# Kernel tuning notes

Measured on AMD Instinct MI355X. Metric: run time of the kernel, lower is better.

The kernel has to match this reference:

```python
import jax, jax.numpy as jnp
import numpy as np

N_HEAD = 16
D_HEAD = 64  # d_model=1024 // n_head=16


def setup_inputs() -> dict:
    key = jax.random.key(0)
    ks = jax.random.split(key, 8)
    B, S, D = 2, 2048, 1024
    scale = 1.0 / np.sqrt(D)
    return {
        "q": jax.random.normal(ks[0], (B, S, D), jnp.float32),
        "k": jax.random.normal(ks[1], (B, S, D), jnp.float32),
        "v": jax.random.normal(ks[2], (B, S, D), jnp.float32),
        "w_q": jax.random.normal(ks[3], (D, D), jnp.float32) * scale,
        "w_k": jax.random.normal(ks[4], (D, D), jnp.float32) * scale,
        "w_v": jax.random.normal(ks[5], (D, D), jnp.float32) * scale,
        "w_fc": jax.random.normal(ks[6], (D, D), jnp.float32) * scale,
        "b_fc": jnp.zeros((D,), jnp.float32),
    }


def reference(q, k, v, w_q, w_k, w_v, w_fc, b_fc):
    B, Sq, D = q.shape
    # projections (torch Linear: x @ W.T), split into heads -> [B, H, S, Dh]
    def proj(x, w):
        return (x @ w.T).reshape(B, x.shape[1], N_HEAD, D_HEAD).transpose(0, 2, 1, 3)
    qh, kh, vh = proj(q, w_q), proj(k, w_k), proj(v, w_v)
    # scaled dot-product attention with explicit weights (dropout = identity, eval mode)
    scores = jnp.einsum("bhqd,bhkd->bhqk", qh, kh) / jnp.sqrt(jnp.float32(D_HEAD))
    attn = jax.nn.softmax(scores, axis=-1)  # [B, H, Sq, Sk]
    ctx = jnp.einsum("bhqk,bhkd->bhqd", attn, vh)
    ctx = ctx.transpose(0, 2, 1, 3).reshape(B, Sq, D)
    out = ctx @ w_fc.T + b_fc
    return out, attn
```

## Files before the change

kernel.cpp:

```cpp
#include <hip/hip_runtime.h>


using f16   = _Float16;
using f16x4 = __attribute__((ext_vector_type(4))) f16;
using f16x8 = __attribute__((ext_vector_type(8))) f16;
using f32x4 = __attribute__((ext_vector_type(4))) float;

#define MFMA16(a, b, c) __builtin_amdgcn_mfma_f32_16x16x32_f16((a), (b), (c), 0, 0, 0)

__device__ static inline float fexp2(float x) {
#if __has_builtin(__builtin_amdgcn_exp2f)
  return __builtin_amdgcn_exp2f(x);
#else
  return exp2f(x);
#endif
}

#define C1 0.18033688011112042f

#define WAIT_BARRIER(IMM)                                              \
  do {                                                                 \
    asm volatile("s_waitcnt vmcnt(" #IMM ") lgkmcnt(0)" ::: "memory"); \
    __builtin_amdgcn_s_barrier();                                      \
  } while (0)

__device__ static inline void gld16(const void* gptr, void* lptr) {
  __builtin_amdgcn_global_load_lds(
      (const __attribute__((address_space(1))) void*)gptr,
      (__attribute__((address_space(3))) void*)lptr, 16, 0, 0);
}

__device__ static inline unsigned int pack2(float a, float b) {
  union { f16 h[2]; unsigned int u; } x;
  x.h[0] = (f16)a; x.h[1] = (f16)b;
  return x.u;
}

__global__ __launch_bounds__(256) void cast_all(
    const float* __restrict__ q, const float* __restrict__ k,
    const float* __restrict__ v, const float* __restrict__ wq,
    const float* __restrict__ wk, const float* __restrict__ wv,
    const float* __restrict__ wfc, f16* __restrict__ ws) {
  int i = blockIdx.x * 256 + threadIdx.x;
  const float* src;
  f16* dst;
  int li;
  if (i < 3145728) {
    if (i < 1048576)      { src = q; dst = ws;            li = i; }
    else if (i < 2097152) { src = k; dst = ws + 4194304;  li = i - 1048576; }
    else                  { src = v; dst = ws + 8388608;  li = i - 2097152; }
  } else {
    int j = i - 3145728;
    int wsel = j >> 18;
    src = (wsel == 0) ? wq : (wsel == 1) ? wk : (wsel == 2) ? wv : wfc;
    dst = ws + 12582912 + wsel * 1048576;
    li = j & 262143;
  }
  float4 x = ((const float4*)src)[li];
  f16x4 y;
  y[0] = (f16)x.x; y[1] = (f16)x.y; y[2] = (f16)x.z; y[3] = (f16)x.w;
  ((f16x4*)dst)[li] = y;
}

template <int MODE, int BN>
__global__ __launch_bounds__(256) void gemm_bt(
    const f16* __restrict__ A0, const f16* __restrict__ W0,
    const float* __restrict__ bias, void* __restrict__ Cout) {
  constexpr int FJ = BN / 32;
  __shared__ unsigned short XA[8192];
  __shared__ unsigned short WB2[BN * 64];
  int tid = threadIdx.x;
  int w = tid >> 6, l = tid & 63, lq = l & 15, g = l >> 4;
  int nb3 = blockIdx.x * BN, mb = blockIdx.y * 128;
  int wsel = (MODE == 4) ? (nb3 >> 10) : 0;
  int nb = (MODE == 4) ? (nb3 & 1023) : nb3;
  const f16* A = (MODE == 4) ? A0 + (size_t)wsel * 4194304 : A0;
  const f16* W = (MODE == 4) ? W0 + (size_t)wsel * 1048576 : W0;
  bool swapR = (MODE == 4) && (wsel == 2);
  int wi = w >> 1, wj = w & 1;

  f32x4 acc[4][FJ];
#pragma unroll
  for (int i = 0; i < 4; i++)
#pragma unroll
    for (int j = 0; j < FJ; j++) acc[i][j] = (f32x4){0.f, 0.f, 0.f, 0.f};

  char* Xb = (char*)XA;
  char* Wb = (char*)WB2;
  int row = tid >> 3;
  int c = (tid & 7) ^ (row & 7);
  const f16* Asrc = A + (size_t)(mb + row) * 1024 + c * 8;
  const f16* Wsrc = W + (size_t)(nb + row) * 1024 + c * 8;

  for (int k0 = 0; k0 < 1024; k0 += 64) {
#pragma unroll
    for (int i2 = 0; i2 < 4; i2++)
      gld16(Asrc + k0 + i2 * 32 * 1024, Xb + i2 * 4096 + w * 1024);
#pragma unroll
    for (int i2 = 0; i2 < BN / 32; i2++)
      gld16(Wsrc + k0 + i2 * 32 * 1024, Wb + i2 * 4096 + w * 1024);
    __syncthreads();

    const char* at = swapR ? Wb : Xb;
    const char* bt = swapR ? Xb : Wb;

    f16x8 bfr[FJ][2];
#pragma unroll
    for (int f = 0; f < FJ; f++) {
      int r = wj * (BN / 2) + f * 16 + lq;
      int sw = (r & 7) << 4;
      bfr[f][0] = *(const f16x8*)(bt + r * 128 + ((g * 16) ^ sw));
      bfr[f][1] = *(const f16x8*)(bt + r * 128 + ((64 + g * 16) ^ sw));
    }
#pragma unroll
    for (int fi = 0; fi < 4; fi++) {
      int r = wi * 64 + fi * 16 + lq;
      int sw = (r & 7) << 4;
      f16x8 a0 = *(const f16x8*)(at + r * 128 + ((g * 16) ^ sw));
      f16x8 a1 = *(const f16x8*)(at + r * 128 + ((64 + g * 16) ^ sw));
#pragma unroll
      for (int fj = 0; fj < FJ; fj++) {
        acc[fi][fj] = MFMA16(a0, bfr[fj][0], acc[fi][fj]);
        acc[fi][fj] = MFMA16(a1, bfr[fj][1], acc[fi][fj]);
      }
    }
    __syncthreads();
  }

#pragma unroll
  for (int fi = 0; fi < 4; fi++) {
#pragma unroll
    for (int fj = 0; fj < FJ; fj++) {
#pragma unroll
      for (int jj = 0; jj < 4; jj++) {
        float v = acc[fi][fj][jj];
        int iG = (swapR ? nb : mb) + wi * 64 + fi * 16 + g * 4 + jj;
        int jG = (swapR ? mb : nb) + wj * (BN / 2) + fj * 16 + lq;
        if constexpr (MODE == 3) {
          int m2 = iG, n2 = jG;
          ((float*)Cout)[(size_t)m2 * 1024 + n2] = v + bias[n2];
        } else {
          f16* dstb = (f16*)Cout + (size_t)wsel * 4194304;
          if (!swapR) {
            int m2 = iG, n2 = jG;
            size_t dst = (size_t)((m2 >> 11) * 16 + (n2 >> 6)) * 131072 +
                         (size_t)(m2 & 2047) * 64 + (n2 & 63);
            dstb[dst] = (f16)v;
          } else {
            int n2 = iG, m2 = jG;
            size_t dst = (size_t)((m2 >> 11) * 1024 + n2) * 2048 + (m2 & 2047);
            dstb[dst] = (f16)v;
          }
        }
      }
    }
  }
}

__global__ __launch_bounds__(256, 2) void attn_fused(
    const f16* __restrict__ qh, const f16* __restrict__ kh,
    const f16* __restrict__ vt, float* __restrict__ attn,
    f16* __restrict__ ctx) {
  __shared__ unsigned short Kl[3][4096];
  __shared__ unsigned short Vl[3][4096];
  __shared__ unsigned short Pl[16384];
  int tid = threadIdx.x;
  int w = tid >> 6, l = tid & 63, lq = l & 15, g = l >> 4;

  int bid = blockIdx.x;
  int xcd = bid & 7, j = bid >> 3;
  int bh = xcd * 4 + (j >> 4);
  int qt = j & 15;

  const f16* qbase = qh + (size_t)(bh * 2048 + qt * 128 + w * 32 + lq) * 64;
  f16x8 qf[2][2];
#pragma unroll
  for (int f = 0; f < 2; f++) {
    qf[f][0] = *(const f16x8*)(qbase + f * 16 * 64 + g * 8);
    qf[f][1] = *(const f16x8*)(qbase + f * 16 * 64 + 32 + g * 8);
  }
  asm volatile("s_waitcnt vmcnt(0)" ::: "memory");

  char* Kb = (char*)Kl;
  char* Vb = (char*)Vl;
  char* Pw = (char*)Pl + w * 8192;

  int row = tid >> 3;
  int c = (tid & 7) ^ (row & 7);
  const f16* ksrc = kh + (size_t)bh * 131072 + (size_t)row * 64 + c * 8;
  const f16* vsrc = vt + (size_t)bh * 131072 + (size_t)row * 2048 + c * 8;

  int swq = (lq & 7) << 4;

#define KISSUE(i, b_)                                               \
  do {                                                              \
    const f16* kp_ = ksrc + (size_t)(i) * 4096;                     \
    char* kb_ = Kb + (b_) * 8192;                                   \
    gld16(kp_, kb_ + w * 1024);                                     \
    gld16(kp_ + 2048, kb_ + 4096 + w * 1024);                       \
  } while (0)
#define VISSUE(i, b_)                                               \
  do {                                                              \
    const f16* vp_ = vsrc + (size_t)(i) * 64;                       \
    char* vb_ = Vb + (b_) * 8192;                                   \
    gld16(vp_, vb_ + w * 1024);                                     \
    gld16(vp_ + 32 * 2048, vb_ + 4096 + w * 1024);                  \
  } while (0)

  float ls[2] = {0.f, 0.f};
  KISSUE(0, 0);
  WAIT_BARRIER(0);
  for (int t = 0; t < 32; t++) {
    if (t < 31) KISSUE(t + 1, (t + 1) & 1);
    const char* KbC = Kb + (t & 1) * 8192;
#pragma unroll
    for (int cf = 0; cf < 4; cf++) {
      int kr = cf * 16 + lq;
      int sw = (kr & 7) << 4;
      f16x8 ka  = *(const f16x8*)(KbC + kr * 128 + ((g * 16) ^ sw));
      f16x8 kb2 = *(const f16x8*)(KbC + kr * 128 + ((64 + g * 16) ^ sw));
#pragma unroll
      for (int f = 0; f < 2; f++) {
        f32x4 s = (f32x4){0.f, 0.f, 0.f, 0.f};
        s = MFMA16(ka, qf[f][0], s);
        s = MFMA16(kb2, qf[f][1], s);
        ls[f] += fexp2(s[0] * C1) + fexp2(s[1] * C1) +
                 fexp2(s[2] * C1) + fexp2(s[3] * C1);
      }
    }
    WAIT_BARRIER(0);
  }
  float linv[2];
#pragma unroll
  for (int f = 0; f < 2; f++) {
    float t2 = ls[f];
    t2 += __shfl_xor(t2, 16);
    t2 += __shfl_xor(t2, 32);
    linv[f] = 1.0f / t2;
  }

  f32x4 acc[2][4];
#pragma unroll
  for (int f = 0; f < 2; f++)
#pragma unroll
    for (int i = 0; i < 4; i++) acc[f][i] = (f32x4){0.f, 0.f, 0.f, 0.f};

  float* attnw =
      attn + ((size_t)bh * 2048 + qt * 128 + w * 32) * 2048;

  int rsub = l >> 5;
  int c4 = (l & 31) * 4;
  int sb = c4 * 2;
  int shalf = sb & 128;
  int slocal = sb & 127;

  KISSUE(0, 0); VISSUE(0, 0);
  KISSUE(1, 1); VISSUE(1, 1);
  WAIT_BARRIER(4);
  int bc = 0;
  for (int t = 0; t < 32; t++) {
    int bn = bc + 2; if (bn >= 3) bn -= 3;
    if (t + 2 < 32) { KISSUE(t + 2, bn); VISSUE(t + 2, bn); }
    const char* KbC = Kb + bc * 8192;
    const char* VbC = Vb + bc * 8192;
    int hb = (t & 1) * 128;

#pragma unroll
    for (int cf = 0; cf < 4; cf++) {
      int kr = cf * 16 + lq;
      int sw = (kr & 7) << 4;
      f16x8 ka  = *(const f16x8*)(KbC + kr * 128 + ((g * 16) ^ sw));
      f16x8 kb2 = *(const f16x8*)(KbC + kr * 128 + ((64 + g * 16) ^ sw));
      int k0 = cf * 16 + g * 4;
#pragma unroll
      for (int f = 0; f < 2; f++) {
        f32x4 s = (f32x4){0.f, 0.f, 0.f, 0.f};
        s = MFMA16(ka, qf[f][0], s);
        s = MFMA16(kb2, qf[f][1], s);
        float e0 = fexp2(s[0] * C1) * linv[f];
        float e1 = fexp2(s[1] * C1) * linv[f];
        float e2 = fexp2(s[2] * C1) * linv[f];
        float e3 = fexp2(s[3] * C1) * linv[f];
        char* Pr = Pw + (f * 16 + lq) * 256 + hb;
        *(unsigned int*)(Pr + ((k0 * 2) ^ swq))       = pack2(e0, e1);
        *(unsigned int*)(Pr + (((k0 + 2) * 2) ^ swq)) = pack2(e2, e3);
      }
    }

    {
      f16x8 pb[2][2];
#pragma unroll
      for (int f = 0; f < 2; f++) {
        char* Pr = Pw + (f * 16 + lq) * 256 + hb;
        pb[f][0] = *(const f16x8*)(Pr + ((g * 16) ^ swq));
        pb[f][1] = *(const f16x8*)(Pr + ((64 + g * 16) ^ swq));
      }
#pragma unroll
      for (int af = 0; af < 4; af++) {
        int vr = af * 16 + lq;
        int sv = (vr & 7) << 4;
        f16x8 va0 = *(const f16x8*)(VbC + vr * 128 + ((g * 16) ^ sv));
        f16x8 va1 = *(const f16x8*)(VbC + vr * 128 + ((64 + g * 16) ^ sv));
#pragma unroll
        for (int f = 0; f < 2; f++) {
          acc[f][af] = MFMA16(va0, pb[f][0], acc[f][af]);
          acc[f][af] = MFMA16(va1, pb[f][1], acc[f][af]);
        }
      }
    }

    if (t & 1) {
      float* abase = attnw + (t - 1) * 64 + c4;
#pragma unroll
      for (int i = 0; i < 16; i++) {
        int r = i * 2 + rsub;
        f16x4 pv = *(const f16x4*)(Pw + r * 256 + shalf +
                                   (slocal ^ ((r & 7) << 4)));
        float4 o = {(float)pv[0], (float)pv[1], (float)pv[2], (float)pv[3]};
        *(float4*)(abase + (size_t)r * 2048) = o;
      }
    }

    if (t == 0)      { WAIT_BARRIER(4);  }
    else if (t >= 30){ WAIT_BARRIER(16); }
    else             { WAIT_BARRIER(20); }
    bc = (bc == 2) ? 0 : bc + 1;
  }

#pragma unroll
  for (int f = 0; f < 2; f++) {
    char* Pr = Pw + (f * 16 + lq) * 256;
#pragma unroll
    for (int af = 0; af < 4; af++) {
#pragma unroll
      for (int jj = 0; jj < 4; jj += 2) {
        int dh0 = af * 16 + g * 4 + jj;
        *(unsigned int*)(Pr + ((dh0 * 2) ^ swq)) =
            pack2(acc[f][af][jj], acc[f][af][jj + 1]);
      }
    }
  }
  {
    int q2 = l >> 1, cc = l & 1;
    int swr = (q2 & 7) << 4;
    int b = bh >> 4, h = bh & 15;
    f16* crow =
        ctx + ((size_t)b * 2048 + qt * 128 + w * 32 + q2) * 1024 + h * 64;
#pragma unroll
    for (int t2 = 0; t2 < 4; t2++) {
      f16x8 v2 = *(const f16x8*)(Pw + q2 * 256 + ((cc * 64 + t2 * 16) ^ swr));
      *(f16x8*)(crow + cc * 32 + t2 * 8) = v2;
    }
  }
#undef KISSUE
#undef VISSUE
}

extern "C" void kernel_launch(void* const* d_in, const int* in_sizes, int n_in,
                              void* d_out, int out_size, void* d_ws,
                              size_t ws_size, hipStream_t stream) {
  (void)in_sizes; (void)n_in; (void)out_size; (void)ws_size;
  const float* q   = (const float*)d_in[0];
  const float* k   = (const float*)d_in[1];
  const float* v   = (const float*)d_in[2];
  const float* wq  = (const float*)d_in[3];
  const float* wk  = (const float*)d_in[4];
  const float* wv  = (const float*)d_in[5];
  const float* wfc = (const float*)d_in[6];
  const float* bfc = (const float*)d_in[7];

  f16* ws = (f16*)d_ws;
  f16* qf   = ws;
  f16* wqf  = ws + 12582912;
  f16* wfcf = ws + 15728640;
  f16* qhp  = ws + 16777216;
  f16* khp  = ws + 20971520;
  f16* vtp  = ws + 25165824;
  f16* ctxp = ws + 29360128;

  float* outp  = (float*)d_out;
  float* attnp = outp + 4194304;

  cast_all<<<16384, 256, 0, stream>>>(q, k, v, wq, wk, wv, wfc, ws);
  gemm_bt<4, 128><<<dim3(24, 32), 256, 0, stream>>>(qf, wqf, nullptr, qhp);
  attn_fused<<<512, 256, 0, stream>>>(qhp, khp, vtp, attnp, ctxp);
  gemm_bt<3, 64><<<dim3(16, 32), 256, 0, stream>>>(ctxp, wfcf, bfc, outp);
}
```

Measured before the change: 274.9 us.

## Rebalance K/V prefetch depth across passes and write attention weights every tile

The row-sum pass moves from double-buffered K with prefetch distance one to a three-slot ring with distance two. The P·V pass drops to double-buffered K/V with distance one. The per-wave P scratch shrinks to one 64-column tile, so attention weights are written to global every iteration instead of every other one. This cuts LDS use per block and adds latency hiding in the first pass, but it reduces prefetch slack in the second, heavier pass and leaves less store batching.

```diff
diff --git a/kernel.cpp b/kernel.cpp
--- a/kernel.cpp
+++ b/kernel.cpp
@@ -162,8 +162,8 @@
     const f16* __restrict__ vt, float* __restrict__ attn,
     f16* __restrict__ ctx) {
   __shared__ unsigned short Kl[3][4096];
-  __shared__ unsigned short Vl[3][4096];
-  __shared__ unsigned short Pl[16384];
+  __shared__ unsigned short Vl[2][4096];
+  __shared__ unsigned short Pl[8192];
   int tid = threadIdx.x;
   int w = tid >> 6, l = tid & 63, lq = l & 15, g = l >> 4;
 
@@ -183,7 +183,7 @@
 
   char* Kb = (char*)Kl;
   char* Vb = (char*)Vl;
-  char* Pw = (char*)Pl + w * 8192;
+  char* Pw = (char*)Pl + w * 4096;
 
   int row = tid >> 3;
   int c = (tid & 7) ^ (row & 7);
@@ -209,26 +209,32 @@
 
   float ls[2] = {0.f, 0.f};
   KISSUE(0, 0);
-  WAIT_BARRIER(0);
-  for (int t = 0; t < 32; t++) {
-    if (t < 31) KISSUE(t + 1, (t + 1) & 1);
-    const char* KbC = Kb + (t & 1) * 8192;
-#pragma unroll
-    for (int cf = 0; cf < 4; cf++) {
-      int kr = cf * 16 + lq;
-      int sw = (kr & 7) << 4;
-      f16x8 ka  = *(const f16x8*)(KbC + kr * 128 + ((g * 16) ^ sw));
-      f16x8 kb2 = *(const f16x8*)(KbC + kr * 128 + ((64 + g * 16) ^ sw));
-#pragma unroll
-      for (int f = 0; f < 2; f++) {
-        f32x4 s = (f32x4){0.f, 0.f, 0.f, 0.f};
-        s = MFMA16(ka, qf[f][0], s);
-        s = MFMA16(kb2, qf[f][1], s);
-        ls[f] += fexp2(s[0] * C1) + fexp2(s[1] * C1) +
-                 fexp2(s[2] * C1) + fexp2(s[3] * C1);
-      }
-    }
-    WAIT_BARRIER(0);
+  KISSUE(1, 1);
+  WAIT_BARRIER(2);
+  {
+    int bc = 0;
+    for (int t = 0; t < 32; t++) {
+      int bn = bc + 2; if (bn >= 3) bn -= 3;
+      if (t + 2 < 32) KISSUE(t + 2, bn);
+      const char* KbC = Kb + bc * 8192;
+#pragma unroll
+      for (int cf = 0; cf < 4; cf++) {
+        int kr = cf * 16 + lq;
+        int sw = (kr & 7) << 4;
+        f16x8 ka  = *(const f16x8*)(KbC + kr * 128 + ((g * 16) ^ sw));
+        f16x8 kb2 = *(const f16x8*)(KbC + kr * 128 + ((64 + g * 16) ^ sw));
+#pragma unroll
+        for (int f = 0; f < 2; f++) {
+          f32x4 s = (f32x4){0.f, 0.f, 0.f, 0.f};
+          s = MFMA16(ka, qf[f][0], s);
+          s = MFMA16(kb2, qf[f][1], s);
+          ls[f] += fexp2(s[0] * C1) + fexp2(s[1] * C1) +
+                   fexp2(s[2] * C1) + fexp2(s[3] * C1);
+        }
+      }
+      if (t < 30) { WAIT_BARRIER(2); } else { WAIT_BARRIER(0); }
+      bc = (bc == 2) ? 0 : bc + 1;
+    }
   }
   float linv[2];
 #pragma unroll
@@ -245,25 +251,22 @@
 #pragma unroll
     for (int i = 0; i < 4; i++) acc[f][i] = (f32x4){0.f, 0.f, 0.f, 0.f};
 
+  int sr_sub = l >> 4;
+  int sc = (l & 15) * 4;
   float* attnw =
       attn + ((size_t)bh * 2048 + qt * 128 + w * 32) * 2048;
 
-  int rsub = l >> 5;
-  int c4 = (l & 31) * 4;
-  int sb = c4 * 2;
-  int shalf = sb & 128;
-  int slocal = sb & 127;
-
-  KISSUE(0, 0); VISSUE(0, 0);
-  KISSUE(1, 1); VISSUE(1, 1);
-  WAIT_BARRIER(4);
-  int bc = 0;
+  KISSUE(0, 0);
+  VISSUE(0, 0);
+  WAIT_BARRIER(0);
   for (int t = 0; t < 32; t++) {
-    int bn = bc + 2; if (bn >= 3) bn -= 3;
-    if (t + 2 < 32) { KISSUE(t + 2, bn); VISSUE(t + 2, bn); }
-    const char* KbC = Kb + bc * 8192;
-    const char* VbC = Vb + bc * 8192;
-    int hb = (t & 1) * 128;
+    int kt = t * 64;
+    const char* KbC = Kb + (t & 1) * 8192;
+    const char* VbC = Vb + (t & 1) * 8192;
+    if (t < 31) {
+      KISSUE(t + 1, (t + 1) & 1);
+      VISSUE(t + 1, (t + 1) & 1);
+    }
 
 #pragma unroll
     for (int cf = 0; cf < 4; cf++) {
@@ -281,7 +284,7 @@
         float e1 = fexp2(s[1] * C1) * linv[f];
         float e2 = fexp2(s[2] * C1) * linv[f];
         float e3 = fexp2(s[3] * C1) * linv[f];
-        char* Pr = Pw + (f * 16 + lq) * 256 + hb;
+        char* Pr = Pw + (f * 16 + lq) * 128;
         *(unsigned int*)(Pr + ((k0 * 2) ^ swq))       = pack2(e0, e1);
         *(unsigned int*)(Pr + (((k0 + 2) * 2) ^ swq)) = pack2(e2, e3);
       }
@@ -291,7 +294,7 @@
       f16x8 pb[2][2];
 #pragma unroll
       for (int f = 0; f < 2; f++) {
-        char* Pr = Pw + (f * 16 + lq) * 256 + hb;
+        char* Pr = Pw + (f * 16 + lq) * 128;
         pb[f][0] = *(const f16x8*)(Pr + ((g * 16) ^ swq));
         pb[f][1] = *(const f16x8*)(Pr + ((64 + g * 16) ^ swq));
       }
@@ -309,27 +312,20 @@
       }
     }
 
-    if (t & 1) {
-      float* abase = attnw + (t - 1) * 64 + c4;
-#pragma unroll
-      for (int i = 0; i < 16; i++) {
-        int r = i * 2 + rsub;
-        f16x4 pv = *(const f16x4*)(Pw + r * 256 + shalf +
-                                   (slocal ^ ((r & 7) << 4)));
-        float4 o = {(float)pv[0], (float)pv[1], (float)pv[2], (float)pv[3]};
-        *(float4*)(abase + (size_t)r * 2048) = o;
-      }
-    }
-
-    if (t == 0)      { WAIT_BARRIER(4);  }
-    else if (t >= 30){ WAIT_BARRIER(16); }
-    else             { WAIT_BARRIER(20); }
-    bc = (bc == 2) ? 0 : bc + 1;
+#pragma unroll
+    for (int i = 0; i < 8; i++) {
+      int r = i * 4 + sr_sub;
+      f16x4 pv = *(const f16x4*)(Pw + r * 128 + ((sc * 2) ^ ((r & 7) << 4)));
+      float4 o = {(float)pv[0], (float)pv[1], (float)pv[2], (float)pv[3]};
+      *(float4*)(attnw + (size_t)r * 2048 + kt + sc) = o;
+    }
+
+    WAIT_BARRIER(8);
   }
 
 #pragma unroll
   for (int f = 0; f < 2; f++) {
-    char* Pr = Pw + (f * 16 + lq) * 256;
+    char* Pr = Pw + (f * 16 + lq) * 128;
 #pragma unroll
     for (int af = 0; af < 4; af++) {
 #pragma unroll
@@ -348,7 +344,7 @@
         ctx + ((size_t)b * 2048 + qt * 128 + w * 32 + q2) * 1024 + h * 64;
 #pragma unroll
     for (int t2 = 0; t2 < 4; t2++) {
-      f16x8 v2 = *(const f16x8*)(Pw + q2 * 256 + ((cc * 64 + t2 * 16) ^ swr));
+      f16x8 v2 = *(const f16x8*)(Pw + q2 * 128 + ((cc * 64 + t2 * 16) ^ swr));
       *(f16x8*)(crow + cc * 32 + t2 * 8) = v2;
     }
   }
```

Measured after the change: 278.5 us. No clear change (+1.3%).
